# Kernel optimization log

Measured on AMD Instinct MI355X. Metric: run time of the kernel, lower is better.

## Reference

```python
import jax, jax.numpy as jnp
import numpy as np

B, C, H, W = 4, 128, 64, 64
D_STATE, D_CONV, EXPAND = 16, 4, 2
D_INNER = EXPAND * C
DT_RANK = (C + 15) // 16  # ceil(d_model/16) = 8
PS = 4                    # patch_size chosen since H%4==0 and W%4==0
L = H * W


def _gelu(x):
    return jax.nn.gelu(x, approximate=False)  # torch nn.GELU default = exact erf


def _dwconv2d(x, w, b):
    y = jax.lax.conv_general_dilated(x, w, (1, 1), 'SAME',
        dimension_numbers=('NCHW', 'OIHW', 'NCHW'), feature_group_count=x.shape[1])
    return y + b[None, :, None, None]


def setup_inputs():
    key = jax.random.key(0)
    k = jax.random.split(key, 16)
    n = lambda i, s, sc=0.02: jax.random.normal(k[i], s, jnp.float32) * sc
    A_log = jnp.log(jnp.broadcast_to(jnp.arange(1, D_STATE + 1, dtype=jnp.float32), (D_INNER, D_STATE)))
    return {
        'x': jax.random.normal(k[0], (B, C, H, W), jnp.float32),
        'pe': n(1, (L, C), 0.02),
        'norm_g': jnp.ones(C), 'norm_b': jnp.zeros(C),
        'conv1_w': n(2, (C, 1, 3, 3), 0.1), 'conv1_b': jnp.zeros(C),
        'ca1_w': n(3, (C // 4, C), 0.1), 'ca2_w': n(4, (C, C // 4), 0.1),
        'conv2_w': n(5, (C, 1, 3, 3), 0.1), 'conv2_b': jnp.zeros(C),
        'head_w': n(6, (1, C), 0.1), 'head_b': jnp.zeros(1),
        'in_proj_w': n(7, (2 * D_INNER, C)),
        'conv1d_w': n(8, (D_INNER, D_CONV), 0.2), 'conv1d_b': jnp.zeros(D_INNER),
        'x_proj_w': n(9, (DT_RANK + 2 * D_STATE, D_INNER)),
        'dt_proj_w': n(10, (D_INNER, DT_RANK), 0.5),
        'dt_proj_b': jnp.full((D_INNER,), -4.6),  # softplus^-1(~0.01)
        'A_log': A_log, 'D': jnp.ones(D_INNER),
        'out_proj_w': n(11, (C, D_INNER)),
    }


def reference(x, pe, norm_g, norm_b, conv1_w, conv1_b, ca1_w, ca2_w, conv2_w, conv2_b,
              head_w, head_b, in_proj_w, conv1d_w, conv1d_b, x_proj_w, dt_proj_w,
              dt_proj_b, A_log, D, out_proj_w):
    # Dynamic_Adaptive_Scan fallback path (DCNv3Function is None): x_adapted == x.
    # (dw_conv/offset outputs are dead code in that path; offset weights are zero-init.)
    x_adapted = x  # (B,C,H,W)

    # ---- CNNScoreMap ----
    feat = _gelu(_dwconv2d(x_adapted, conv1_w, conv1_b))          # depthwise 3x3 (groups=C)
    ca = feat.mean((2, 3))                                        # global avg pool -> (B,C)
    ca = jax.nn.sigmoid(jnp.maximum(ca @ ca1_w.T, 0.0) @ ca2_w.T)
    feat = feat * ca[:, :, None, None]
    feat = _gelu(_dwconv2d(feat, conv2_w, conv2_b))
    scores = jax.nn.sigmoid(jnp.einsum('bchw,oc->bohw', feat, head_w)[:, 0] + head_b[0])
    pv = jnp.var(x_adapted, axis=1, ddof=1)                       # torch.var is unbiased
    final_scores = 0.7 * scores + 0.3 * jax.nn.sigmoid(pv * 10.0)  # (B,H,W)

    # ---- patch pooling (patch_size=4) + descending importance sort ----
    Hp, Wp = H // PS, W // PS
    sm = final_scores.reshape(B, Hp, PS, Wp, PS).mean((2, 4)).reshape(B, Hp * Wp)
    idx = jnp.argsort(-sm, axis=1)                                # (B, num_patches)
    p_y, p_x = idx // Wp, idx % Wp
    offs_y = jnp.repeat(jnp.arange(PS), PS)
    offs_x = jnp.tile(jnp.arange(PS), PS)
    pix_y = p_y[:, :, None] * PS + offs_y[None, None, :]
    pix_x = p_x[:, :, None] * PS + offs_x[None, None, :]
    order = (pix_y * W + pix_x).reshape(B, L)                     # pixel scan order

    # ---- reorder tokens, add PE, LayerNorm ----
    pe_re = pe[order]                                             # (B,L,C)
    x_re = jnp.take_along_axis(x_adapted.reshape(B, C, L),
                               jnp.broadcast_to(order[:, None, :], (B, C, L)), axis=2)
    x1 = x_re.transpose(0, 2, 1) + pe_re                          # (B,L,C)
    mu = x1.mean(-1, keepdims=True)
    var = ((x1 - mu) ** 2).mean(-1, keepdims=True)
    x1n = (x1 - mu) * jax.lax.rsqrt(var + 1e-5) * norm_g + norm_b

    # ---- Mamba block ----
    xz = x1n @ in_proj_w.T                                        # (B,L,2*Di)
    xm, z = xz[..., :D_INNER], xz[..., D_INNER:]
    xp = jnp.pad(xm.transpose(0, 2, 1), ((0, 0), (0, 0), (D_CONV - 1, 0)))  # causal pad
    xc = jax.lax.conv_general_dilated(xp, conv1d_w[:, None, :], (1,), 'VALID',
        dimension_numbers=('NCH', 'OIH', 'NCH'), feature_group_count=D_INNER)
    xc = jax.nn.silu(xc + conv1d_b[None, :, None]).transpose(0, 2, 1)       # (B,L,Di)
    dbc = xc @ x_proj_w.T                                         # (B,L,dt_rank+2*Ds)
    dt_low = dbc[..., :DT_RANK]
    Bc = dbc[..., DT_RANK:DT_RANK + D_STATE]
    Cc = dbc[..., DT_RANK + D_STATE:]
    dt = jax.nn.softplus(dt_low @ dt_proj_w.T + dt_proj_b)        # (B,L,Di)
    A = -jnp.exp(A_log)                                           # (Di,Ds)
    dA = jnp.exp(dt[..., None] * A)                               # (B,L,Di,Ds)
    dBx = dt[..., None] * Bc[:, :, None, :] * xc[..., None]       # (B,L,Di,Ds)

    def step(h, inp):
        dA_t, dBx_t, C_t = inp
        h = dA_t * h + dBx_t
        return h, jnp.einsum('bds,bs->bd', h, C_t)

    h0 = jnp.zeros((B, D_INNER, D_STATE), xc.dtype)
    _, ys = jax.lax.scan(step, h0, (dA.transpose(1, 0, 2, 3),
                                    dBx.transpose(1, 0, 2, 3),
                                    Cc.transpose(1, 0, 2)))
    y = ys.transpose(1, 0, 2) + D * xc                            # (B,L,Di)
    y = y * jax.nn.silu(z)
    out_m = y @ out_proj_w.T                                      # (B,L,C)

    # ---- inverse reorder back to image layout ----
    inv = jnp.argsort(order, axis=1)
    out_flat = jnp.take_along_axis(out_m.transpose(0, 2, 1),
                                   jnp.broadcast_to(inv[:, None, :], (B, C, L)), axis=2)
    return out_flat.reshape(B, C, H, W)
```

## Files before the change

kernel.cpp:

```cpp
#include <hip/hip_runtime.h>
#include <math.h>

#define BB   4
#define NCH  128
#define TCH  32

__device__ __forceinline__ float sigm(float x){ return 1.0f/(1.0f + __expf(-x)); }
__device__ __forceinline__ float gelu_(float x){ return 0.5f*x*(1.0f + erff(x*0.7071067811865475f)); }
__device__ __forceinline__ float silu_(float x){ return x*sigm(x); }
__device__ __forceinline__ float softplus_(float x){ return fmaxf(x,0.0f) + log1pf(__expf(-fabsf(x))); }


__global__ void k_conv1(const float* __restrict__ x, const float* __restrict__ w,
                        const float* __restrict__ bias, float* __restrict__ out){
  int idx = blockIdx.x*256 + threadIdx.x;
  int wx = idx & 63, hy = (idx>>6)&63, c = (idx>>12)&127;
  const float* xp = x + (idx & ~4095);
  float acc = 0.f;
  #pragma unroll
  for (int dy=-1; dy<=1; ++dy){
    int hh = hy+dy; if ((unsigned)hh > 63u) continue;
    #pragma unroll
    for (int dx=-1; dx<=1; ++dx){
      int ww = wx+dx; if ((unsigned)ww > 63u) continue;
      acc += xp[hh*64+ww] * w[c*9 + (dy+1)*3 + (dx+1)];
    }
  }
  out[idx] = gelu_(acc + bias[c]);
}

__global__ void k_chanmean(const float* __restrict__ feat, float* __restrict__ ca_in){
  int bc = blockIdx.x; int tid = threadIdx.x;
  const float* p = feat + (size_t)bc*4096;
  float s = 0.f;
  for (int i=tid; i<4096; i+=256) s += p[i];
  __shared__ float red[256];
  red[tid] = s; __syncthreads();
  for (int st=128; st>0; st>>=1){ if (tid<st) red[tid]+=red[tid+st]; __syncthreads(); }
  if (tid==0) ca_in[bc] = red[0]*(1.0f/4096.0f);
}

__global__ void k_camlp(const float* __restrict__ ca_in, const float* __restrict__ w1,
                        const float* __restrict__ w2, float* __restrict__ ca){
  int b = blockIdx.x; int tid = threadIdx.x;
  __shared__ float cin[128], hid[32];
  cin[tid] = ca_in[b*128+tid];
  __syncthreads();
  if (tid < 32){
    float a = 0.f;
    for (int c=0;c<128;++c) a += cin[c]*w1[tid*128+c];
    hid[tid] = fmaxf(a, 0.f);
  }
  __syncthreads();
  float a = 0.f;
  #pragma unroll
  for (int j=0;j<32;++j) a += hid[j]*w2[tid*32+j];
  ca[b*128+tid] = sigm(a);
}

__global__ void k_conv2(const float* __restrict__ f1, const float* __restrict__ w,
                        const float* __restrict__ bias, const float* __restrict__ ca,
                        float* __restrict__ out){
  int idx = blockIdx.x*256 + threadIdx.x;
  int wx = idx & 63, hy = (idx>>6)&63, c = (idx>>12)&127;
  const float* xp = f1 + (idx & ~4095);
  float acc = 0.f;
  #pragma unroll
  for (int dy=-1; dy<=1; ++dy){
    int hh = hy+dy; if ((unsigned)hh > 63u) continue;
    #pragma unroll
    for (int dx=-1; dx<=1; ++dx){
      int ww = wx+dx; if ((unsigned)ww > 63u) continue;
      acc += xp[hh*64+ww] * w[c*9 + (dy+1)*3 + (dx+1)];
    }
  }
  out[idx] = gelu_(ca[idx>>12]*acc + bias[c]);
}

__global__ void k_final(const float* __restrict__ feat2, const float* __restrict__ x,
                        const float* __restrict__ hw, const float* __restrict__ hb,
                        float* __restrict__ finalv){
  int gid = blockIdx.x*256 + threadIdx.x;
  int b = gid >> 12, pix = gid & 4095;
  const float* f = feat2 + (size_t)b*128*4096 + pix;
  float s1 = 0.f;
  for (int c=0;c<128;++c) s1 += f[c*4096]*hw[c];
  float sc = sigm(s1 + hb[0]);
  const float* xp = x + (size_t)b*128*4096 + pix;
  float su=0.f, sq=0.f;
  for (int c=0;c<128;++c){ float v = xp[c*4096]; su += v; sq += v*v; }
  float mu = su*(1.0f/128.0f);
  float pv = (sq - 128.0f*mu*mu)*(1.0f/127.0f);
  finalv[gid] = 0.7f*sc + 0.3f*sigm(pv*10.0f);
}

__global__ void k_order(const float* __restrict__ finalv, int* __restrict__ order,
                        int* __restrict__ inv){
  int b = blockIdx.x; int p = threadIdx.x;
  __shared__ float sm[256];
  __shared__ int ord[256];
  int py = p >> 4, px = p & 15;
  const float* fv = finalv + b*4096;
  float s = 0.f;
  #pragma unroll
  for (int oy=0; oy<4; ++oy)
    #pragma unroll
    for (int ox=0; ox<4; ++ox)
      s += fv[(py*4+oy)*64 + px*4+ox];
  sm[p] = s;
  __syncthreads();
  float v = sm[p];
  int r = 0;
  for (int j=0;j<256;++j){
    float u = sm[j];
    r += (u > v) || (u == v && j < p);
  }
  ord[r] = p;
  __syncthreads();
  int patch = ord[p];
  int base = (patch>>4)*4*64 + (patch&15)*4;
  #pragma unroll
  for (int j=0;j<16;++j){
    int pix = base + (j>>2)*64 + (j&3);
    int l = p*16 + j;
    order[b*4096 + l] = pix;
    inv[b*4096 + pix] = l;
  }
}


__global__ void k_transpose(const float* __restrict__ x, float* __restrict__ xT){
  __shared__ float tile[32][33];
  int b = blockIdx.z; int c0 = blockIdx.y*32; int l0 = blockIdx.x*32;
  int tx = threadIdx.x, ty = threadIdx.y;
  #pragma unroll
  for (int j=0;j<4;++j)
    tile[ty+j*8][tx] = x[((size_t)(b*128 + c0+ty+j*8))*4096 + l0+tx];
  __syncthreads();
  #pragma unroll
  for (int j=0;j<4;++j)
    xT[((size_t)(b*4096 + l0+ty+j*8))*128 + c0+tx] = tile[tx][ty+j*8];
}

__global__ void k_gatherln(const float* __restrict__ xT, const float* __restrict__ pe,
                           const int* __restrict__ order, const float* __restrict__ g,
                           const float* __restrict__ bb, float* __restrict__ x1n){
  int n = blockIdx.x; int c = threadIdx.x;
  int b = n >> 12;
  int pix = order[n];
  float v = xT[((size_t)(b*4096+pix))*128 + c] + pe[pix*128 + c];
  float s1 = v, s2 = v*v;
  #pragma unroll
  for (int m=1; m<64; m<<=1){
    s1 += __shfl_xor(s1, m, 64);
    s2 += __shfl_xor(s2, m, 64);
  }
  __shared__ float ws1[2], ws2[2];
  int wid = c >> 6;
  if ((c & 63) == 0){ ws1[wid]=s1; ws2[wid]=s2; }
  __syncthreads();
  float t1 = ws1[0]+ws1[1], t2 = ws2[0]+ws2[1];
  float mu = t1*(1.0f/128.0f);
  float var = t2*(1.0f/128.0f) - mu*mu;
  x1n[(size_t)n*128 + c] = (v-mu)*rsqrtf(var+1e-5f)*g[c] + bb[c];
}

__global__ __launch_bounds__(256) void k_gemm(const float* __restrict__ A,
    const float* __restrict__ Bw, float* __restrict__ C, int M, int N, int K){
  __shared__ float As[16*132];
  __shared__ float Bs[16*68];
  int m0 = blockIdx.x*128, n0 = blockIdx.y*64;
  int tid = threadIdx.x;
  int tx = tid & 15;
  int ty = tid >> 4;
  int am = tid >> 1;
  int ak = (tid & 1) * 8;
  int bn = tid >> 2;
  int bk = (tid & 3) * 4;
  float acc[8][4] = {};
  for (int k0 = 0; k0 < K; k0 += 16){
    float4 a0 = *(const float4*)&A[(size_t)(m0+am)*K + k0 + ak];
    float4 a1 = *(const float4*)&A[(size_t)(m0+am)*K + k0 + ak + 4];
    float4 b0 = *(const float4*)&Bw[(size_t)(n0+bn)*K + k0 + bk];
    As[(ak+0)*132+am]=a0.x; As[(ak+1)*132+am]=a0.y;
    As[(ak+2)*132+am]=a0.z; As[(ak+3)*132+am]=a0.w;
    As[(ak+4)*132+am]=a1.x; As[(ak+5)*132+am]=a1.y;
    As[(ak+6)*132+am]=a1.z; As[(ak+7)*132+am]=a1.w;
    Bs[(bk+0)*68+bn]=b0.x; Bs[(bk+1)*68+bn]=b0.y;
    Bs[(bk+2)*68+bn]=b0.z; Bs[(bk+3)*68+bn]=b0.w;
    __syncthreads();
    #pragma unroll
    for (int kk=0;kk<16;++kk){
      float4 av0 = *(const float4*)&As[kk*132 + ty*8];
      float4 av1 = *(const float4*)&As[kk*132 + ty*8 + 4];
      float4 bv  = *(const float4*)&Bs[kk*68 + tx*4];
      float a8[8] = {av0.x,av0.y,av0.z,av0.w,av1.x,av1.y,av1.z,av1.w};
      float b4[4] = {bv.x,bv.y,bv.z,bv.w};
      #pragma unroll
      for (int i=0;i<8;++i)
        #pragma unroll
        for (int j=0;j<4;++j)
          acc[i][j] = fmaf(a8[i], b4[j], acc[i][j]);
    }
    __syncthreads();
  }
  #pragma unroll
  for (int i=0;i<8;++i){
    float4 v; v.x=acc[i][0]; v.y=acc[i][1]; v.z=acc[i][2]; v.w=acc[i][3];
    *(float4*)&C[(size_t)(m0+ty*8+i)*N + n0+tx*4] = v;
  }
}

__global__ __launch_bounds__(256) void k_conv1d(const float* __restrict__ xz,
    const float* __restrict__ w, const float* __restrict__ bias, float* __restrict__ xc){
  __shared__ float S[35*256];
  int n0 = blockIdx.x*32;
  int b = n0 >> 12; int l0 = n0 & 4095;
  int tid = threadIdx.x;
  for (int i = tid; i < 35*64; i += 256){
    int r = i >> 6, cq = i & 63;
    int ll = l0 - 3 + r;
    float4 v = {0.f,0.f,0.f,0.f};
    if (ll >= 0) v = *(const float4*)&xz[((size_t)(b*4096 + ll))*512 + cq*4];
    *(float4*)&S[r*256 + cq*4] = v;
  }
  __syncthreads();
  int d = tid;
  float4 wv = *(const float4*)&w[d*4];
  float bv = bias[d];
  float s0=S[0*256+d], s1=S[1*256+d], s2=S[2*256+d];
  for (int r=0;r<32;++r){
    float s3 = S[(r+3)*256+d];
    float acc = fmaf(wv.x,s0,fmaf(wv.y,s1,fmaf(wv.z,s2,fmaf(wv.w,s3,bv))));
    xc[(size_t)(n0+r)*256 + d] = silu_(acc);
    s0=s1; s1=s2; s2=s3;
  }
}

__global__ __launch_bounds__(256) void k_scan1(const float* __restrict__ xc,
    const float* __restrict__ wxp, const float* __restrict__ wdt,
    const float* __restrict__ bdt, float* __restrict__ dbc40,
    float* __restrict__ P, float* __restrict__ hend){
  int b = blockIdx.x >> 7; int ch = blockIdx.x & 127; int tid = threadIdx.x;
  int nbase = b*4096 + ch*TCH;
  __shared__ float xcs[TCH*260];
  __shared__ float Ws[40*66];
  __shared__ float Ds[TCH*44];
  for (int i = tid; i < TCH*64; i += 256){
    int r = i >> 6, kq = i & 63;
    float4 v = *(const float4*)&xc[(size_t)(nbase+r)*256 + kq*4];
    *(float4*)&xcs[r*260 + kq*4] = v;
  }
  int tq = tid >> 3;
  int oo = tid & 7;
  float pacc[5] = {0.f,0.f,0.f,0.f,0.f};
  for (int h = 0; h < 4; ++h){
    __syncthreads();
    for (int i = tid; i < 40*16; i += 256){
      int o = i >> 4, kq = i & 15;
      *(float4*)&Ws[o*66 + kq*4] = *(const float4*)&wxp[(size_t)o*256 + h*64 + kq*4];
    }
    __syncthreads();
    #pragma unroll
    for (int kt = 0; kt < 16; ++kt){
      float4 xv = *(const float4*)&xcs[tq*260 + h*64 + kt*4];
      #pragma unroll
      for (int j = 0; j < 5; ++j){
        float4 wv = *(const float4*)&Ws[(oo+8*j)*66 + kt*4];
        pacc[j] = fmaf(xv.x,wv.x, fmaf(xv.y,wv.y, fmaf(xv.z,wv.z, fmaf(xv.w,wv.w, pacc[j]))));
      }
    }
  }
  __syncthreads();
  #pragma unroll
  for (int j = 0; j < 5; ++j) Ds[tq*44 + oo + 8*j] = pacc[j];
  __syncthreads();
  for (int i = tid; i < TCH*40; i += 256){
    int r = i/40, o = i - r*40;
    dbc40[(size_t)(nbase+r)*40 + o] = Ds[r*44 + o];
  }
  int d = tid;
  float4 w0 = *(const float4*)&wdt[d*8];
  float4 w1 = *(const float4*)&wdt[d*8+4];
  float bdv = bdt[d];
  float h_[16];
  #pragma unroll
  for (int s=0;s<16;++s) h_[s]=0.f;
  float Etot = 1.f;
  for (int t = 0; t < TCH; ++t){
    const float* lo = &Ds[t*44];
    float a = bdv;
    a = fmaf(lo[0],w0.x,a); a = fmaf(lo[1],w0.y,a);
    a = fmaf(lo[2],w0.z,a); a = fmaf(lo[3],w0.w,a);
    a = fmaf(lo[4],w1.x,a); a = fmaf(lo[5],w1.y,a);
    a = fmaf(lo[6],w1.z,a); a = fmaf(lo[7],w1.w,a);
    float dtv = softplus_(a);
    float xcv = xcs[t*260 + d];
    float dtx = dtv * xcv;
    float e1 = __expf(-dtv);
    Etot *= e1;
    float ap = 1.f;
    #pragma unroll
    for (int s=0;s<16;++s){
      ap *= e1;
      h_[s] = fmaf(ap, h_[s], dtx*Ds[t*44 + 8 + s]);
    }
  }
  size_t base = ((size_t)((b*256+d)*NCH + ch))*16;
  float pw = 1.f;
  #pragma unroll
  for (int s=0;s<16;++s){ pw *= Etot; P[base+s] = pw; hend[base+s] = h_[s]; }
}

__global__ void k_scan2(const float* __restrict__ P, const float* __restrict__ hend,
                        float* __restrict__ hstart){
  int gid = blockIdx.x*256 + threadIdx.x;
  int s = gid & 15; int bd = gid >> 4;
  size_t base = (size_t)bd*(NCH*16) + s;
  float hs = 0.f;
  for (int ch=0; ch<NCH; ++ch){
    hstart[base + ch*16] = hs;
    hs = fmaf(P[base + ch*16], hs, hend[base + ch*16]);
  }
}

__global__ __launch_bounds__(256) void k_scan3(const float* __restrict__ xc,
    const float* __restrict__ dbc40, const float* __restrict__ wdt,
    const float* __restrict__ bdt, const float* __restrict__ hstart,
    const float* __restrict__ Dv, const float* __restrict__ xz, float* __restrict__ y){
  int b = blockIdx.x >> 7; int ch = blockIdx.x & 127; int d = threadIdx.x;
  __shared__ float Bs[TCH*16], Cs[TCH*16], Dl[TCH*8];
  int nbase = b*4096 + ch*TCH;
  for (int i=d; i<TCH*16; i+=256){
    size_t r = (size_t)(nbase + (i>>4))*40;
    Bs[i] = dbc40[r + 8 + (i&15)];
    Cs[i] = dbc40[r + 24 + (i&15)];
  }
  {
    int t = d >> 3, r = d & 7;
    Dl[d] = dbc40[(size_t)(nbase+t)*40 + r];
  }
  __syncthreads();
  float4 w0 = *(const float4*)&wdt[d*8];
  float4 w1 = *(const float4*)&wdt[d*8+4];
  float bdv = bdt[d];
  float h_[16];
  size_t hb = ((size_t)((b*256+d)*NCH + ch))*16;
  #pragma unroll
  for (int s=0;s<16;++s) h_[s] = hstart[hb+s];
  float Dd = Dv[d];
  for (int t=0; t<TCH; ++t){
    size_t n = (size_t)(nbase + t);
    const float* lo = &Dl[t*8];
    float a = bdv;
    a = fmaf(lo[0],w0.x,a); a = fmaf(lo[1],w0.y,a);
    a = fmaf(lo[2],w0.z,a); a = fmaf(lo[3],w0.w,a);
    a = fmaf(lo[4],w1.x,a); a = fmaf(lo[5],w1.y,a);
    a = fmaf(lo[6],w1.z,a); a = fmaf(lo[7],w1.w,a);
    float dtv = softplus_(a);
    float xcv = xc[n*256 + d];
    float dtx = dtv * xcv;
    float e1 = __expf(-dtv);
    float ap = 1.f;
    float yv = 0.f;
    #pragma unroll
    for (int s=0;s<16;++s){
      ap *= e1;
      h_[s] = fmaf(ap, h_[s], dtx*Bs[t*16+s]);
      yv = fmaf(h_[s], Cs[t*16+s], yv);
    }
    float zv = xz[n*512 + 256 + d];
    y[n*256 + d] = (yv + Dd*xcv) * silu_(zv);
  }
}

__global__ __launch_bounds__(256) void k_scatter(const float* __restrict__ out_m,
    const int* __restrict__ inv, float* __restrict__ out){
  __shared__ float T[128*65];
  __shared__ int ls[64];
  int b = blockIdx.x >> 6;
  int m0 = (blockIdx.x & 63) * 64;
  int tid = threadIdx.x;
  if (tid < 64) ls[tid] = inv[b*4096 + m0 + tid];
  __syncthreads();
  for (int i = tid; i < 64*128; i += 256){
    int mm = i >> 7, c = i & 127;
    T[c*65 + mm] = out_m[((size_t)(b*4096 + ls[mm]))*128 + c];
  }
  __syncthreads();
  for (int i = tid; i < 128*64; i += 256){
    int c = i >> 6, mm = i & 63;
    out[((size_t)(b*128 + c))*4096 + m0 + mm] = T[c*65 + mm];
  }
}

extern "C" void kernel_launch(void* const* d_in, const int* in_sizes, int n_in,
                              void* d_out, int out_size, void* d_ws, size_t ws_size,
                              hipStream_t stream) {
  const float* x         = (const float*)d_in[0];
  const float* pe        = (const float*)d_in[1];
  const float* norm_g    = (const float*)d_in[2];
  const float* norm_b    = (const float*)d_in[3];
  const float* conv1_w   = (const float*)d_in[4];
  const float* conv1_b   = (const float*)d_in[5];
  const float* ca1_w     = (const float*)d_in[6];
  const float* ca2_w     = (const float*)d_in[7];
  const float* conv2_w   = (const float*)d_in[8];
  const float* conv2_b   = (const float*)d_in[9];
  const float* head_w    = (const float*)d_in[10];
  const float* head_b    = (const float*)d_in[11];
  const float* in_proj_w = (const float*)d_in[12];
  const float* conv1d_w  = (const float*)d_in[13];
  const float* conv1d_b  = (const float*)d_in[14];
  const float* x_proj_w  = (const float*)d_in[15];
  const float* dt_proj_w = (const float*)d_in[16];
  const float* dt_proj_b = (const float*)d_in[17];
  const float* Dv        = (const float*)d_in[19];
  const float* out_proj_w= (const float*)d_in[20];

  float* ws = (float*)d_ws;
  size_t o = 0;
  float* feat1 = ws + o; o += 2097152;
  float* feat2 = ws + o; o += 2097152;
  float* ca_in = ws + o; o += 512;
  float* ca    = ws + o; o += 512;
  float* finalv= ws + o; o += 16384;
  int*   order = (int*)(ws + o); o += 16384;
  int*   inv   = (int*)(ws + o); o += 16384;
  float* xz    = ws + o; o += 8388608;
  float* xc    = ws + o; o += 4194304;
  float* dbc40 = ws + o; o += 655360;
  float* ybuf  = ws + o; o += 4194304;
  float* hstart= ws + o; o += 2097152;

  float* xT    = feat1;
  float* x1n   = feat2;
  float* Pbuf  = feat1;
  float* hendb = feat2;
  float* out_m = xz;

  k_conv1   <<<8192, 256, 0, stream>>>(x, conv1_w, conv1_b, feat1);
  k_chanmean<<<512, 256, 0, stream>>>(feat1, ca_in);
  k_camlp   <<<BB, 128, 0, stream>>>(ca_in, ca1_w, ca2_w, ca);
  k_conv2   <<<8192, 256, 0, stream>>>(feat1, conv2_w, conv2_b, ca, feat2);
  k_final   <<<64, 256, 0, stream>>>(feat2, x, head_w, head_b, finalv);
  k_order   <<<BB, 256, 0, stream>>>(finalv, order, inv);
  k_transpose<<<dim3(128,4,BB), dim3(32,8), 0, stream>>>(x, xT);
  k_gatherln<<<16384, 128, 0, stream>>>(xT, pe, order, norm_g, norm_b, x1n);
  k_gemm    <<<dim3(128,8), 256, 0, stream>>>(x1n, in_proj_w, xz, 16384, 512, 128);
  k_conv1d  <<<512, 256, 0, stream>>>(xz, conv1d_w, conv1d_b, xc);
  k_scan1   <<<BB*NCH, 256, 0, stream>>>(xc, x_proj_w, dt_proj_w, dt_proj_b, dbc40, Pbuf, hendb);
  k_scan2   <<<64, 256, 0, stream>>>(Pbuf, hendb, hstart);
  k_scan3   <<<BB*NCH, 256, 0, stream>>>(xc, dbc40, dt_proj_w, dt_proj_b, hstart, Dv, xz, ybuf);
  k_gemm    <<<dim3(128,2), 256, 0, stream>>>(ybuf, out_proj_w, out_m, 16384, 128, 256);
  k_scatter <<<256, 256, 0, stream>>>(out_m, inv, (float*)d_out);
}
```

Measured before the change: 316.6 us.

## Halve scan chunk length, store per-chunk decay scalar, break scan dependency chains

The chunked selective scan now uses 256 chunks of 16 steps instead of 128 chunks of 32, doubling the number of scan blocks so more of the device is busy. Instead of writing 16 decay powers per chunk, scan1 stores one total-decay scalar, and scan2 rebuilds each power by binary exponentiation, which shrinks that buffer. The per-step decay powers are built as a shallow product tree instead of a serial chain, the y reduction is split into four partial sums, and loads from shared memory are vectorised. In exchange scan2 runs a serial loop twice as long, hend now reuses the y buffer before scan3 overwrites it, and occupancy hints were added.

```diff
diff --git a/kernel.cpp b/kernel.cpp
--- a/kernel.cpp
+++ b/kernel.cpp
@@ -2,8 +2,8 @@
 #include <math.h>
 
 #define BB   4
-#define NCH  128
-#define TCH  32
+#define NCH  256
+#define TCH  16
 
 __device__ __forceinline__ float sigm(float x){ return 1.0f/(1.0f + __expf(-x)); }
 __device__ __forceinline__ float gelu_(float x){ return 0.5f*x*(1.0f + erff(x*0.7071067811865475f)); }
@@ -237,11 +237,11 @@
   }
 }
 
-__global__ __launch_bounds__(256) void k_scan1(const float* __restrict__ xc,
+__global__ __launch_bounds__(256,4) void k_scan1(const float* __restrict__ xc,
     const float* __restrict__ wxp, const float* __restrict__ wdt,
     const float* __restrict__ bdt, float* __restrict__ dbc40,
-    float* __restrict__ P, float* __restrict__ hend){
-  int b = blockIdx.x >> 7; int ch = blockIdx.x & 127; int tid = threadIdx.x;
+    float* __restrict__ Etot_g, float* __restrict__ hend){
+  int b = blockIdx.x >> 8; int ch = blockIdx.x & 255; int tid = threadIdx.x;
   int nbase = b*4096 + ch*TCH;
   __shared__ float xcs[TCH*260];
   __shared__ float Ws[40*66];
@@ -251,33 +251,35 @@
     float4 v = *(const float4*)&xc[(size_t)(nbase+r)*256 + kq*4];
     *(float4*)&xcs[r*260 + kq*4] = v;
   }
-  int tq = tid >> 3;
-  int oo = tid & 7;
-  float pacc[5] = {0.f,0.f,0.f,0.f,0.f};
+  int tq = tid >> 4;
+  int oo = tid & 15;
+  float pacc[3] = {0.f,0.f,0.f};
   for (int h = 0; h < 4; ++h){
     __syncthreads();
     for (int i = tid; i < 40*16; i += 256){
-      int o = i >> 4, kq = i & 15;
-      *(float4*)&Ws[o*66 + kq*4] = *(const float4*)&wxp[(size_t)o*256 + h*64 + kq*4];
+      int o2 = i >> 4, kq = i & 15;
+      *(float4*)&Ws[o2*66 + kq*4] = *(const float4*)&wxp[(size_t)o2*256 + h*64 + kq*4];
     }
     __syncthreads();
     #pragma unroll
     for (int kt = 0; kt < 16; ++kt){
       float4 xv = *(const float4*)&xcs[tq*260 + h*64 + kt*4];
-      #pragma unroll
-      for (int j = 0; j < 5; ++j){
-        float4 wv = *(const float4*)&Ws[(oo+8*j)*66 + kt*4];
-        pacc[j] = fmaf(xv.x,wv.x, fmaf(xv.y,wv.y, fmaf(xv.z,wv.z, fmaf(xv.w,wv.w, pacc[j]))));
-      }
+      float4 wa = *(const float4*)&Ws[oo*66 + kt*4];
+      float4 wb = *(const float4*)&Ws[(oo+16)*66 + kt*4];
+      float4 wc = *(const float4*)&Ws[((oo&7)+32)*66 + kt*4];
+      pacc[0] = fmaf(xv.x,wa.x, fmaf(xv.y,wa.y, fmaf(xv.z,wa.z, fmaf(xv.w,wa.w, pacc[0]))));
+      pacc[1] = fmaf(xv.x,wb.x, fmaf(xv.y,wb.y, fmaf(xv.z,wb.z, fmaf(xv.w,wb.w, pacc[1]))));
+      pacc[2] = fmaf(xv.x,wc.x, fmaf(xv.y,wc.y, fmaf(xv.z,wc.z, fmaf(xv.w,wc.w, pacc[2]))));
     }
   }
   __syncthreads();
-  #pragma unroll
-  for (int j = 0; j < 5; ++j) Ds[tq*44 + oo + 8*j] = pacc[j];
+  Ds[tq*44 + oo]      = pacc[0];
+  Ds[tq*44 + oo + 16] = pacc[1];
+  if (oo < 8) Ds[tq*44 + oo + 32] = pacc[2];
   __syncthreads();
   for (int i = tid; i < TCH*40; i += 256){
-    int r = i/40, o = i - r*40;
-    dbc40[(size_t)(nbase+r)*40 + o] = Ds[r*44 + o];
+    int r = i/40, o2 = i - r*40;
+    dbc40[(size_t)(nbase+r)*40 + o2] = Ds[r*44 + o2];
   }
   int d = tid;
   float4 w0 = *(const float4*)&wdt[d*8];
@@ -286,59 +288,89 @@
   float h_[16];
   #pragma unroll
   for (int s=0;s<16;++s) h_[s]=0.f;
-  float Etot = 1.f;
+  float Et = 1.f;
   for (int t = 0; t < TCH; ++t){
     const float* lo = &Ds[t*44];
-    float a = bdv;
-    a = fmaf(lo[0],w0.x,a); a = fmaf(lo[1],w0.y,a);
-    a = fmaf(lo[2],w0.z,a); a = fmaf(lo[3],w0.w,a);
-    a = fmaf(lo[4],w1.x,a); a = fmaf(lo[5],w1.y,a);
-    a = fmaf(lo[6],w1.z,a); a = fmaf(lo[7],w1.w,a);
+    float4 l0 = *(const float4*)&lo[0];
+    float4 l1 = *(const float4*)&lo[4];
+    float a0 = fmaf(l0.x,w0.x, fmaf(l0.y,w0.y, fmaf(l0.z,w0.z, fmaf(l0.w,w0.w, bdv))));
+    float a1 = fmaf(l1.x,w1.x, fmaf(l1.y,w1.y, fmaf(l1.z,w1.z, l1.w*w1.w)));
+    float a = a0 + a1;
     float dtv = softplus_(a);
-    float xcv = xcs[t*260 + d];
-    float dtx = dtv * xcv;
     float e1 = __expf(-dtv);
-    Etot *= e1;
-    float ap = 1.f;
-    #pragma unroll
-    for (int s=0;s<16;++s){
-      ap *= e1;
-      h_[s] = fmaf(ap, h_[s], dtx*Ds[t*44 + 8 + s]);
-    }
-  }
-  size_t base = ((size_t)((b*256+d)*NCH + ch))*16;
-  float pw = 1.f;
-  #pragma unroll
-  for (int s=0;s<16;++s){ pw *= Etot; P[base+s] = pw; hend[base+s] = h_[s]; }
-}
-
-__global__ void k_scan2(const float* __restrict__ P, const float* __restrict__ hend,
+    float dtx = dtv * xcs[t*260 + d];
+    Et *= e1;
+    float e2=e1*e1, e4=e2*e2, e8=e4*e4;
+    float a3=e2*e1, a5=e4*e1, a6=e4*e2, a7=e4*a3;
+    float4 b0 = *(const float4*)&lo[8];
+    float4 b1 = *(const float4*)&lo[12];
+    float4 b2 = *(const float4*)&lo[16];
+    float4 b3 = *(const float4*)&lo[20];
+    h_[0]  = fmaf(e1,    h_[0],  dtx*b0.x);
+    h_[1]  = fmaf(e2,    h_[1],  dtx*b0.y);
+    h_[2]  = fmaf(a3,    h_[2],  dtx*b0.z);
+    h_[3]  = fmaf(e4,    h_[3],  dtx*b0.w);
+    h_[4]  = fmaf(a5,    h_[4],  dtx*b1.x);
+    h_[5]  = fmaf(a6,    h_[5],  dtx*b1.y);
+    h_[6]  = fmaf(a7,    h_[6],  dtx*b1.z);
+    h_[7]  = fmaf(e8,    h_[7],  dtx*b1.w);
+    h_[8]  = fmaf(e8*e1, h_[8],  dtx*b2.x);
+    h_[9]  = fmaf(e8*e2, h_[9],  dtx*b2.y);
+    h_[10] = fmaf(e8*a3, h_[10], dtx*b2.z);
+    h_[11] = fmaf(e8*e4, h_[11], dtx*b2.w);
+    h_[12] = fmaf(e8*a5, h_[12], dtx*b3.x);
+    h_[13] = fmaf(e8*a6, h_[13], dtx*b3.y);
+    h_[14] = fmaf(e8*a7, h_[14], dtx*b3.z);
+    h_[15] = fmaf(e8*e8, h_[15], dtx*b3.w);
+  }
+  size_t idx = (size_t)((b*256+d)*NCH + ch);
+  Etot_g[idx] = Et;
+  size_t hb = idx*16;
+  #pragma unroll
+  for (int s=0;s<16;s+=4){
+    float4 v; v.x=h_[s]; v.y=h_[s+1]; v.z=h_[s+2]; v.w=h_[s+3];
+    *(float4*)&hend[hb+s] = v;
+  }
+}
+
+__global__ void k_scan2(const float* __restrict__ Etot_g, const float* __restrict__ hend,
                         float* __restrict__ hstart){
   int gid = blockIdx.x*256 + threadIdx.x;
   int s = gid & 15; int bd = gid >> 4;
+  int e = s + 1;
   size_t base = (size_t)bd*(NCH*16) + s;
+  const float* Ep = Etot_g + (size_t)bd*NCH;
   float hs = 0.f;
   for (int ch=0; ch<NCH; ++ch){
     hstart[base + ch*16] = hs;
-    hs = fmaf(P[base + ch*16], hs, hend[base + ch*16]);
-  }
-}
-
-__global__ __launch_bounds__(256) void k_scan3(const float* __restrict__ xc,
+    float E = Ep[ch];
+    float E2=E*E, E4=E2*E2, E8=E4*E4, E16=E8*E8;
+    float p = 1.f;
+    if (e & 1)  p *= E;
+    if (e & 2)  p *= E2;
+    if (e & 4)  p *= E4;
+    if (e & 8)  p *= E8;
+    if (e & 16) p *= E16;
+    hs = fmaf(p, hs, hend[base + ch*16]);
+  }
+}
+
+__global__ __launch_bounds__(256,4) void k_scan3(const float* __restrict__ xc,
     const float* __restrict__ dbc40, const float* __restrict__ wdt,
     const float* __restrict__ bdt, const float* __restrict__ hstart,
     const float* __restrict__ Dv, const float* __restrict__ xz, float* __restrict__ y){
-  int b = blockIdx.x >> 7; int ch = blockIdx.x & 127; int d = threadIdx.x;
+  int b = blockIdx.x >> 8; int ch = blockIdx.x & 255; int d = threadIdx.x;
   __shared__ float Bs[TCH*16], Cs[TCH*16], Dl[TCH*8];
   int nbase = b*4096 + ch*TCH;
-  for (int i=d; i<TCH*16; i+=256){
+  {
+    int i = d;
     size_t r = (size_t)(nbase + (i>>4))*40;
     Bs[i] = dbc40[r + 8 + (i&15)];
     Cs[i] = dbc40[r + 24 + (i&15)];
-  }
-  {
-    int t = d >> 3, r = d & 7;
-    Dl[d] = dbc40[(size_t)(nbase+t)*40 + r];
+    if (d < TCH*8){
+      int t = d >> 3, rr = d & 7;
+      Dl[d] = dbc40[(size_t)(nbase+t)*40 + rr];
+    }
   }
   __syncthreads();
   float4 w0 = *(const float4*)&wdt[d*8];
@@ -347,30 +379,53 @@
   float h_[16];
   size_t hb = ((size_t)((b*256+d)*NCH + ch))*16;
   #pragma unroll
-  for (int s=0;s<16;++s) h_[s] = hstart[hb+s];
+  for (int s=0;s<16;s+=4){
+    float4 v = *(const float4*)&hstart[hb+s];
+    h_[s]=v.x; h_[s+1]=v.y; h_[s+2]=v.z; h_[s+3]=v.w;
+  }
   float Dd = Dv[d];
   for (int t=0; t<TCH; ++t){
     size_t n = (size_t)(nbase + t);
     const float* lo = &Dl[t*8];
-    float a = bdv;
-    a = fmaf(lo[0],w0.x,a); a = fmaf(lo[1],w0.y,a);
-    a = fmaf(lo[2],w0.z,a); a = fmaf(lo[3],w0.w,a);
-    a = fmaf(lo[4],w1.x,a); a = fmaf(lo[5],w1.y,a);
-    a = fmaf(lo[6],w1.z,a); a = fmaf(lo[7],w1.w,a);
+    float4 l0 = *(const float4*)&lo[0];
+    float4 l1 = *(const float4*)&lo[4];
+    float a0 = fmaf(l0.x,w0.x, fmaf(l0.y,w0.y, fmaf(l0.z,w0.z, fmaf(l0.w,w0.w, bdv))));
+    float a1 = fmaf(l1.x,w1.x, fmaf(l1.y,w1.y, fmaf(l1.z,w1.z, l1.w*w1.w)));
+    float a = a0 + a1;
     float dtv = softplus_(a);
+    float e1 = __expf(-dtv);
     float xcv = xc[n*256 + d];
     float dtx = dtv * xcv;
-    float e1 = __expf(-dtv);
-    float ap = 1.f;
-    float yv = 0.f;
-    #pragma unroll
-    for (int s=0;s<16;++s){
-      ap *= e1;
-      h_[s] = fmaf(ap, h_[s], dtx*Bs[t*16+s]);
-      yv = fmaf(h_[s], Cs[t*16+s], yv);
-    }
+    float e2=e1*e1, e4=e2*e2, e8=e4*e4;
+    float a3=e2*e1, a5=e4*e1, a6=e4*e2, a7=e4*a3;
+    float4 B0 = *(const float4*)&Bs[t*16];
+    float4 B1 = *(const float4*)&Bs[t*16+4];
+    float4 B2 = *(const float4*)&Bs[t*16+8];
+    float4 B3 = *(const float4*)&Bs[t*16+12];
+    float4 C0 = *(const float4*)&Cs[t*16];
+    float4 C1 = *(const float4*)&Cs[t*16+4];
+    float4 C2 = *(const float4*)&Cs[t*16+8];
+    float4 C3 = *(const float4*)&Cs[t*16+12];
+    float y0,y1,y2,y3;
+    h_[0]  = fmaf(e1,    h_[0],  dtx*B0.x); y0 = h_[0]*C0.x;
+    h_[1]  = fmaf(e2,    h_[1],  dtx*B0.y); y1 = h_[1]*C0.y;
+    h_[2]  = fmaf(a3,    h_[2],  dtx*B0.z); y2 = h_[2]*C0.z;
+    h_[3]  = fmaf(e4,    h_[3],  dtx*B0.w); y3 = h_[3]*C0.w;
+    h_[4]  = fmaf(a5,    h_[4],  dtx*B1.x); y0 = fmaf(h_[4],  C1.x, y0);
+    h_[5]  = fmaf(a6,    h_[5],  dtx*B1.y); y1 = fmaf(h_[5],  C1.y, y1);
+    h_[6]  = fmaf(a7,    h_[6],  dtx*B1.z); y2 = fmaf(h_[6],  C1.z, y2);
+    h_[7]  = fmaf(e8,    h_[7],  dtx*B1.w); y3 = fmaf(h_[7],  C1.w, y3);
+    h_[8]  = fmaf(e8*e1, h_[8],  dtx*B2.x); y0 = fmaf(h_[8],  C2.x, y0);
+    h_[9]  = fmaf(e8*e2, h_[9],  dtx*B2.y); y1 = fmaf(h_[9],  C2.y, y1);
+    h_[10] = fmaf(e8*a3, h_[10], dtx*B2.z); y2 = fmaf(h_[10], C2.z, y2);
+    h_[11] = fmaf(e8*e4, h_[11], dtx*B2.w); y3 = fmaf(h_[11], C2.w, y3);
+    h_[12] = fmaf(e8*a5, h_[12], dtx*B3.x); y0 = fmaf(h_[12], C3.x, y0);
+    h_[13] = fmaf(e8*a6, h_[13], dtx*B3.y); y1 = fmaf(h_[13], C3.y, y1);
+    h_[14] = fmaf(e8*a7, h_[14], dtx*B3.z); y2 = fmaf(h_[14], C3.z, y2);
+    h_[15] = fmaf(e8*e8, h_[15], dtx*B3.w); y3 = fmaf(h_[15], C3.w, y3);
+    float yv = (y0+y1)+(y2+y3);
     float zv = xz[n*512 + 256 + d];
-    y[n*256 + d] = (yv + Dd*xcv) * silu_(zv);
+    y[n*256 + d] = fmaf(Dd, xcv, yv) * silu_(zv);
   }
 }
 
@@ -431,12 +486,12 @@
   float* xc    = ws + o; o += 4194304;
   float* dbc40 = ws + o; o += 655360;
   float* ybuf  = ws + o; o += 4194304;
-  float* hstart= ws + o; o += 2097152;
+  float* etot  = ws + o; o += 262144;
 
   float* xT    = feat1;
   float* x1n   = feat2;
-  float* Pbuf  = feat1;
-  float* hendb = feat2;
+  float* hstart= feat1;
+  float* hend  = ybuf;
   float* out_m = xz;
 
   k_conv1   <<<8192, 256, 0, stream>>>(x, conv1_w, conv1_b, feat1);
@@ -449,8 +504,8 @@
   k_gatherln<<<16384, 128, 0, stream>>>(xT, pe, order, norm_g, norm_b, x1n);
   k_gemm    <<<dim3(128,8), 256, 0, stream>>>(x1n, in_proj_w, xz, 16384, 512, 128);
   k_conv1d  <<<512, 256, 0, stream>>>(xz, conv1d_w, conv1d_b, xc);
-  k_scan1   <<<BB*NCH, 256, 0, stream>>>(xc, x_proj_w, dt_proj_w, dt_proj_b, dbc40, Pbuf, hendb);
-  k_scan2   <<<64, 256, 0, stream>>>(Pbuf, hendb, hstart);
+  k_scan1   <<<BB*NCH, 256, 0, stream>>>(xc, x_proj_w, dt_proj_w, dt_proj_b, dbc40, etot, hend);
+  k_scan2   <<<64, 256, 0, stream>>>(etot, hend, hstart);
   k_scan3   <<<BB*NCH, 256, 0, stream>>>(xc, dbc40, dt_proj_w, dt_proj_b, hstart, Dv, xz, ybuf);
   k_gemm    <<<dim3(128,2), 256, 0, stream>>>(ybuf, out_proj_w, out_m, 16384, 128, 256);
   k_scatter <<<256, 256, 0, stream>>>(out_m, inv, (float*)d_out);
```

Result: slower. 339.6 us (+7.3%).
